# Optimization experiments

Hardware: AMD Instinct MI355X
Metric: run time of the kernel (lower is better)

The kernel has to match this reference:

```python
import jax, jax.numpy as jnp
import numpy as np


def setup_inputs() -> dict:
    key = jax.random.key(0)
    k1, k2, k3 = jax.random.split(key, 3)
    B, C_in, H, W = 32, 128, 64, 64
    C_out, KH, KW = 256, 3, 3
    x = jax.random.normal(k1, (B, C_in, H, W), dtype=jnp.float32)
    # kaiming_normal fan_out scale ~ sqrt(2 / (C_out*KH*KW)); plain normal is fine for a numeric reference
    weight = jax.random.normal(k2, (C_out, C_in, KH, KW), dtype=jnp.float32) * (2.0 / (C_out * KH * KW)) ** 0.5
    fan_in = C_in * KH * KW
    bound = 1.0 / (fan_in ** 0.5)
    bias = jax.random.uniform(k3, (C_out,), dtype=jnp.float32, minval=-bound, maxval=bound)
    return {"x": x, "weight": weight, "bias": bias}


def reference(x, weight, bias):
    # Equivalent of unfold (im2col) + matmul + fold with stride=1, padding=1:
    # a standard 2D convolution in NCHW/OIHW layout.
    out = jax.lax.conv_general_dilated(
        x, weight,
        window_strides=(1, 1),
        padding=((1, 1), (1, 1)),
        dimension_numbers=("NCHW", "OIHW", "NCHW"),
    )
    return out + bias[None, :, None, None]
```

## Files before the change

kernel.cpp:

```cpp
#include <hip/hip_runtime.h>

typedef __attribute__((ext_vector_type(4))) int   v4i;
typedef __attribute__((ext_vector_type(8))) short s8;
typedef __attribute__((ext_vector_type(4))) float f32x4;
typedef __attribute__((ext_vector_type(16))) float f32x16;

#define GLB __attribute__((address_space(1)))
#define LDS_AS __attribute__((address_space(3)))

__device__ __forceinline__ unsigned short f2bf(float f) {
  unsigned u = __builtin_bit_cast(unsigned, f);
  return (unsigned short)((u + 0x7fffu + ((u >> 16) & 1u)) >> 16);
}

__global__ void prep(const float* __restrict__ x, const float* __restrict__ w,
                     unsigned int* __restrict__ xw, unsigned short* __restrict__ ww) {
  int t = threadIdx.x;
  if (blockIdx.x >= 2048) {
    int o = (blockIdx.x - 2048) * 256 + t;
    int tap = o >> 15;
    int c   = (o >> 13) & 3;
    int cog = (o >> 10) & 7;
    int kk  = (o >> 9) & 1;
    int lh  = (o >> 8) & 1;
    int l31 = (o >> 3) & 31;
    int e   = o & 7;
    int co = cog * 32 + l31;
    int ci = c * 32 + kk * 16 + lh * 8 + e;
    ww[o] = f2bf(w[(co * 128 + ci) * 9 + tap]);
    return;
  }
  __shared__ float tile[128][65];
  int bid = blockIdx.x;
  int b = bid >> 6, h = bid & 63;
  {
    int wcol4 = (t & 15) * 4, cl = t >> 4;
    const float* src = x + ((size_t)(b * 128) * 64 + h) * 64 + wcol4;
#pragma unroll
    for (int j = 0; j < 8; ++j) {
      int ci = j * 16 + cl;
      f32x4 v = *(const f32x4*)(src + (size_t)ci * 4096);
      tile[ci][wcol4 + 0] = v[0];
      tile[ci][wcol4 + 1] = v[1];
      tile[ci][wcol4 + 2] = v[2];
      tile[ci][wcol4 + 3] = v[3];
    }
  }
  unsigned int* dst = xw + (size_t)((b * 66 + h + 1) * 66) * 64;
  if (t < 128) {
    int col = (t >> 6) ? 65 : 0;
    dst[(size_t)col * 64 + (t & 63)] = 0u;
  }
  if (h == 0 || h == 63) {
    unsigned int* rb = xw + (size_t)(b * 66 + (h == 0 ? 0 : 65)) * 66 * 64;
    for (int j = t; j < 66 * 64; j += 256) rb[j] = 0u;
  }
  __syncthreads();
  {
    int ci2 = (t & 63) * 2, wl = t >> 6;
#pragma unroll
    for (int j = 0; j < 16; ++j) {
      int wcol = j * 4 + wl;
      unsigned p = (unsigned)f2bf(tile[ci2][wcol]) |
                   ((unsigned)f2bf(tile[ci2 + 1][wcol]) << 16);
      dst[(size_t)(wcol + 1) * 64 + (t & 63)] = p;
    }
  }
}

__global__ __launch_bounds__(256, 4) void conv_mfma(
    const unsigned short* __restrict__ xw, const unsigned short* __restrict__ ww,
    const float* __restrict__ bias, float* __restrict__ out) {
  __shared__ unsigned short Xl[204 * 128];
  const int tid = threadIdx.x;
  const int lane = tid & 63;
  const int l31 = lane & 31, lh = lane >> 5;
  const int mw = tid >> 6;
  int bid = blockIdx.x;
  bid = (bid & 7) * 512 + (bid >> 3);
  const int co_t = bid & 1;
  const int pt = bid >> 1;
  const int b = pt >> 6, h0 = pt & 63;
  const unsigned xlb = (unsigned)(unsigned long long)((LDS_AS void*)Xl);

  {
    const char* xbase = (const char*)xw;
#pragma unroll
    for (int it = 0; it < 13; ++it) {
      int s = tid + it * 256;
      if (s < 3264) {
        int q = s >> 4, p = s & 15;
        int u = p ^ (q & 15);
        int rr = q / 68, cc = q - rr * 68;
        if (cc > 65) cc = 65;
        unsigned src = (unsigned)((b * 66 + h0 + rr) * 66 + cc) * 256u + (unsigned)u * 16u;
        __builtin_amdgcn_global_load_lds((const GLB unsigned int*)(xbase + src),
                                         (LDS_AS unsigned int*)&Xl[s * 8], 16, 0, 0);
      }
    }
  }

  f32x16 acc[2];
#pragma unroll
  for (int n = 0; n < 2; ++n)
#pragma unroll
    for (int e = 0; e < 16; ++e) acc[n][e] = 0.f;

  v4i areg[3][2];
  v4i breg[2][4];
  const unsigned abyte = (unsigned)(co_t * 8192 + mw * 2048 + lane * 16);

  #define ALOAD_ASM(slot, step)                                               \
    do {                                                                      \
      unsigned _wo = (unsigned)(step) * 16384u + abyte;                       \
      asm volatile("global_load_dwordx4 %0, %1, %2 offset:0"                  \
                   : "=v"(areg[slot][0]) : "v"(_wo), "s"(ww));                \
      asm volatile("global_load_dwordx4 %0, %1, %2 offset:1024"               \
                   : "=v"(areg[slot][1]) : "v"(_wo), "s"(ww));                \
    } while (0)

  #define BLOAD_ASM(slot, S)                                                  \
    do {                                                                      \
      const int _t = (S) >> 2, _c = (S) & 3;                                  \
      const int _kh = _t / 3, _kw = _t - _kh * 3;                             \
      const int _q0 = _kh * 68 + _kw + l31;                                   \
      const int _xq = (_q0 & 15) ^ lh;             \
      unsigned _a0 = xlb + (unsigned)((_q0 << 8) + (((_c * 4) ^ _xq) << 4));  \
      unsigned _a1 = xlb + (unsigned)((_q0 << 8) + (((_c * 4 + 2) ^ _xq) << 4)); \
      asm volatile("ds_read_b128 %0, %1" : "=v"(breg[slot][0]) : "v"(_a0));   \
      asm volatile("ds_read_b128 %0, %1 offset:8192"                          \
                   : "=v"(breg[slot][1]) : "v"(_a0));                         \
      asm volatile("ds_read_b128 %0, %1" : "=v"(breg[slot][2]) : "v"(_a1));   \
      asm volatile("ds_read_b128 %0, %1 offset:8192"                          \
                   : "=v"(breg[slot][3]) : "v"(_a1));                         \
    } while (0)

  #define KSTEP(S)                                                            \
    do {                                                                      \
      const int _s = (S);                                                     \
      if (_s < 34) ALOAD_ASM((_s + 2) % 3, _s + 2);                           \
      if (_s < 35) BLOAD_ASM((_s + 1) & 1, _s + 1);                           \
      if (_s < 34)                                                            \
        asm volatile("s_waitcnt vmcnt(4) lgkmcnt(4)" ::: "memory");           \
      else if (_s == 34)                                                      \
        asm volatile("s_waitcnt vmcnt(2) lgkmcnt(4)" ::: "memory");           \
      else                                                                    \
        asm volatile("s_waitcnt vmcnt(0) lgkmcnt(0)" ::: "memory");           \
      __builtin_amdgcn_sched_barrier(0);                                      \
      const int _cs = _s % 3, _bs = _s & 1;                                   \
      __builtin_amdgcn_s_setprio(1);                                          \
      acc[0] = __builtin_amdgcn_mfma_f32_32x32x16_bf16(__builtin_bit_cast(s8, areg[_cs][0]), __builtin_bit_cast(s8, breg[_bs][0]), acc[0], 0, 0, 0); \
      acc[1] = __builtin_amdgcn_mfma_f32_32x32x16_bf16(__builtin_bit_cast(s8, areg[_cs][0]), __builtin_bit_cast(s8, breg[_bs][1]), acc[1], 0, 0, 0); \
      acc[0] = __builtin_amdgcn_mfma_f32_32x32x16_bf16(__builtin_bit_cast(s8, areg[_cs][1]), __builtin_bit_cast(s8, breg[_bs][2]), acc[0], 0, 0, 0); \
      acc[1] = __builtin_amdgcn_mfma_f32_32x32x16_bf16(__builtin_bit_cast(s8, areg[_cs][1]), __builtin_bit_cast(s8, breg[_bs][3]), acc[1], 0, 0, 0); \
      __builtin_amdgcn_s_setprio(0);                                          \
    } while (0)

  ALOAD_ASM(0, 0);
  ALOAD_ASM(1, 1);
  asm volatile("s_waitcnt vmcnt(4)" ::: "memory");
  __builtin_amdgcn_sched_barrier(0);
  __builtin_amdgcn_s_barrier();
  BLOAD_ASM(0, 0);

#pragma unroll
  for (int s = 0; s < 36; ++s) KSTEP(s);

#pragma unroll
  for (int rq = 0; rq < 4; ++rq) {
    const int cob = co_t * 128 + mw * 32 + 8 * rq + 4 * lh;
    const f32x4 bi = *(const f32x4*)(bias + cob);
#pragma unroll
    for (int n = 0; n < 2; ++n) {
      const int wc = n * 32 + l31;
      size_t base = ((size_t)(b * 256 + cob) * 64 + h0) * 64 + wc;
#pragma unroll
      for (int e = 0; e < 4; ++e)
        out[base + (size_t)e * 4096] = acc[n][rq * 4 + e] + bi[e];
    }
  }
}

__global__ void conv_naive(const float* __restrict__ x, const float* __restrict__ w,
                           const float* __restrict__ bias, float* __restrict__ out) {
  int i = blockIdx.x * 256 + threadIdx.x;
  int wc = i & 63, h = (i >> 6) & 63, co = (i >> 12) & 255, b = i >> 20;
  float s = bias[co];
  for (int ci = 0; ci < 128; ++ci)
#pragma unroll
    for (int kh = 0; kh < 3; ++kh) {
      int hh = h + kh - 1;
      if ((unsigned)hh >= 64u) continue;
#pragma unroll
      for (int kw = 0; kw < 3; ++kw) {
        int wg = wc + kw - 1;
        if ((unsigned)wg >= 64u) continue;
        s += x[((b * 128 + ci) * 64 + hh) * 64 + wg] *
             w[((co * 128 + ci) * 3 + kh) * 3 + kw];
      }
    }
  out[i] = s;
}

extern "C" void kernel_launch(void* const* d_in, const int* in_sizes, int n_in,
                              void* d_out, int out_size, void* d_ws, size_t ws_size,
                              hipStream_t stream) {
  const float* x    = (const float*)d_in[0];
  const float* w    = (const float*)d_in[1];
  const float* bias = (const float*)d_in[2];
  float* out = (float*)d_out;

  const size_t X_OFF  = 1ull << 20;
  const size_t XBYTES = 32ull * 66 * 66 * 128 * 2;
  const size_t NEED   = X_OFF + XBYTES;

  if (ws_size >= NEED) {
    unsigned short* ww = (unsigned short*)d_ws;
    unsigned short* xq = (unsigned short*)((char*)d_ws + X_OFF);
    hipLaunchKernelGGL(prep, dim3(3200), dim3(256), 0, stream, x, w,
                       (unsigned int*)xq, ww);
    hipLaunchKernelGGL(conv_mfma, dim3(4096), dim3(256), 0, stream, xq, ww, bias, out);
  } else {
    hipLaunchKernelGGL(conv_naive, dim3(131072), dim3(256), 0, stream, x, w, bias, out);
  }
}
```

Baseline: 98.49 us.

## Enlarge conv tile to 256 channels by 256 pixels with double-buffered LDS staging

The MFMA conv kernel now has each 512-thread block compute all 256 output channels for four output rows (256 pixels). Both weights and the input halo slices are staged into a double-buffered LDS ring via direct global-to-LDS loads, one k-tile ahead. Each wave computes a 128x64 sub-tile with 4x2 MFMA accumulators, fed by LDS fragment reads interleaved with the MFMAs. This is meant to raise operand reuse and cut redundant global traffic for weights and inputs. In exchange it uses more registers, a full 128KB of LDS, two barriers per k-step, and only 512 blocks.

```diff
diff --git a/kernel.cpp b/kernel.cpp
--- a/kernel.cpp
+++ b/kernel.cpp
@@ -68,117 +68,151 @@
   }
 }
 
-__global__ __launch_bounds__(256, 4) void conv_mfma(
+__global__ __launch_bounds__(512, 2) void conv_mfma(
     const unsigned short* __restrict__ xw, const unsigned short* __restrict__ ww,
     const float* __restrict__ bias, float* __restrict__ out) {
-  __shared__ unsigned short Xl[204 * 128];
+  __shared__ unsigned short Xl[65536];
   const int tid = threadIdx.x;
   const int lane = tid & 63;
   const int l31 = lane & 31, lh = lane >> 5;
-  const int mw = tid >> 6;
+  const int wid = tid >> 6;
+  const int wm = wid >> 2;
+  const int wn = wid & 3;
   int bid = blockIdx.x;
-  bid = (bid & 7) * 512 + (bid >> 3);
-  const int co_t = bid & 1;
-  const int pt = bid >> 1;
-  const int b = pt >> 6, h0 = pt & 63;
+  bid = (bid & 7) * 64 + (bid >> 3);
+  const int b = bid >> 4, h0 = (bid & 15) << 2;
   const unsigned xlb = (unsigned)(unsigned long long)((LDS_AS void*)Xl);
-
-  {
-    const char* xbase = (const char*)xw;
-#pragma unroll
-    for (int it = 0; it < 13; ++it) {
-      int s = tid + it * 256;
-      if (s < 3264) {
-        int q = s >> 4, p = s & 15;
-        int u = p ^ (q & 15);
-        int rr = q / 68, cc = q - rr * 68;
-        if (cc > 65) cc = 65;
-        unsigned src = (unsigned)((b * 66 + h0 + rr) * 66 + cc) * 256u + (unsigned)u * 16u;
-        __builtin_amdgcn_global_load_lds((const GLB unsigned int*)(xbase + src),
-                                         (LDS_AS unsigned int*)&Xl[s * 8], 16, 0, 0);
+  const char* wwb = (const char*)ww;
+  const char* xqb = (const char*)xw;
+
+  unsigned ia[4], pbx[4];
+#pragma unroll
+  for (int j = 0; j < 4; ++j) {
+    int s = tid + j * 512;
+    int cog = s >> 8, cp = (s >> 7) & 1, kk = (s >> 6) & 1;
+    int lhs = (s >> 5) & 1, l31s = s & 31;
+    ia[j] = (unsigned)((cog * 1024 + kk * 512 + lhs * 256 + l31s * 8) * 2 + cp * 16384);
+    int pix = s & 255, u = s >> 8;
+    int pr = pix >> 6, pc = pix & 63;
+    pbx[j] = (unsigned)(((b * 66 + h0 + pr) * 66 + pc) * 256 + u * 16);
+  }
+
+  #define STAGE(kt)                                                           \
+    do {                                                                      \
+      const int _tap = (kt) >> 1, _ch = (kt) & 1;                             \
+      const unsigned _ka = (unsigned)(_tap * 65536 + _ch * 32768);            \
+      const int _kh = _tap / 3, _kw = _tap - _kh * 3;                         \
+      const unsigned _kb = (unsigned)((_kh * 66 + _kw) * 256 + _ch * 128);    \
+      const int _abh = ((kt) & 1) * 16384;                  \
+      _Pragma("unroll")                                                       \
+      for (int _j = 0; _j < 4; ++_j)                                          \
+        __builtin_amdgcn_global_load_lds(                                     \
+            (const GLB unsigned int*)(wwb + _ka + ia[_j]),                    \
+            (LDS_AS unsigned int*)&Xl[_abh + (tid + _j * 512) * 8], 16, 0, 0);\
+      _Pragma("unroll")                                                       \
+      for (int _j = 0; _j < 4; ++_j)                                          \
+        __builtin_amdgcn_global_load_lds(                                     \
+            (const GLB unsigned int*)(xqb + _kb + pbx[_j]),                   \
+            (LDS_AS unsigned int*)&Xl[32768 + _abh + (tid + _j * 512) * 8],   \
+            16, 0, 0);                                                        \
+    } while (0)
+
+  f32x16 acc[4][2];
+#pragma unroll
+  for (int m = 0; m < 4; ++m)
+#pragma unroll
+    for (int n = 0; n < 2; ++n)
+#pragma unroll
+      for (int e = 0; e < 16; ++e) acc[m][n][e] = 0.f;
+
+  v4i aph[2][4];
+  v4i bph[2][2];
+  const unsigned ard = (unsigned)(wm * 16384 + lane * 16);
+  const unsigned brd = (unsigned)(65536 + lh * 4096 + (wn * 64 + l31) * 16);
+
+  #define APH(sl, p, bo)                                                      \
+    do {                                                                      \
+      unsigned _a = xlb + (bo) + ard + (unsigned)((p) * 1024);                \
+      asm volatile("ds_read_b128 %0, %1"              : "=v"(aph[sl][0]) : "v"(_a)); \
+      asm volatile("ds_read_b128 %0, %1 offset:4096"  : "=v"(aph[sl][1]) : "v"(_a)); \
+      asm volatile("ds_read_b128 %0, %1 offset:8192"  : "=v"(aph[sl][2]) : "v"(_a)); \
+      asm volatile("ds_read_b128 %0, %1 offset:12288" : "=v"(aph[sl][3]) : "v"(_a)); \
+    } while (0)
+
+  #define BPH(sl, p, bo)                                                      \
+    do {                                                                      \
+      unsigned _b = xlb + (bo) + brd + (unsigned)((p) * 8192);                \
+      asm volatile("ds_read_b128 %0, %1"             : "=v"(bph[sl][0]) : "v"(_b)); \
+      asm volatile("ds_read_b128 %0, %1 offset:512"  : "=v"(bph[sl][1]) : "v"(_b)); \
+    } while (0)
+
+  #define MFMA1(d, af, bf) \
+    d = __builtin_amdgcn_mfma_f32_32x32x16_bf16(__builtin_bit_cast(s8, af), \
+                                                __builtin_bit_cast(s8, bf), d, 0, 0, 0)
+  #define MFMA8(sl)                                                           \
+    do {                                                                      \
+      MFMA1(acc[0][0], aph[sl][0], bph[sl][0]);                               \
+      MFMA1(acc[1][0], aph[sl][1], bph[sl][0]);                               \
+      MFMA1(acc[2][0], aph[sl][2], bph[sl][0]);                               \
+      MFMA1(acc[3][0], aph[sl][3], bph[sl][0]);                               \
+      MFMA1(acc[0][1], aph[sl][0], bph[sl][1]);                               \
+      MFMA1(acc[1][1], aph[sl][1], bph[sl][1]);                               \
+      MFMA1(acc[2][1], aph[sl][2], bph[sl][1]);                               \
+      MFMA1(acc[3][1], aph[sl][3], bph[sl][1]);                               \
+    } while (0)
+
+  #define SB __builtin_amdgcn_sched_barrier(0)
+  #define PRIO1 __builtin_amdgcn_s_setprio(1)
+  #define PRIO0 __builtin_amdgcn_s_setprio(0)
+
+  STAGE(0);
+
+#pragma unroll
+  for (int kt = 0; kt < 18; ++kt) {
+    const unsigned bo = (unsigned)((kt & 1) * 32768);
+    if (kt < 17) {
+      STAGE(kt + 1);
+      asm volatile("s_waitcnt vmcnt(8)" ::: "memory");
+    } else {
+      asm volatile("s_waitcnt vmcnt(0)" ::: "memory");
+    }
+    SB;
+    __builtin_amdgcn_s_barrier();
+
+    APH(0, 0, bo); BPH(0, 0, bo);
+    APH(1, 1, bo); BPH(1, 1, bo);
+    asm volatile("s_waitcnt lgkmcnt(6)" ::: "memory");
+    SB; PRIO1; MFMA8(0); PRIO0;
+
+    APH(0, 2, bo); BPH(0, 2, bo);
+    asm volatile("s_waitcnt lgkmcnt(6)" ::: "memory");
+    SB; PRIO1; MFMA8(1); PRIO0;
+
+    APH(1, 3, bo); BPH(1, 3, bo);
+    asm volatile("s_waitcnt lgkmcnt(6)" ::: "memory");
+    SB; PRIO1; MFMA8(0); PRIO0;
+
+    asm volatile("s_waitcnt lgkmcnt(0)" ::: "memory");
+    SB; PRIO1; MFMA8(1); PRIO0;
+    __builtin_amdgcn_s_barrier();
+  }
+
+#pragma unroll
+  for (int m = 0; m < 4; ++m)
+#pragma unroll
+    for (int rq = 0; rq < 4; ++rq) {
+      const int cob = wm * 128 + m * 32 + 8 * rq + 4 * lh;
+      const f32x4 bi = *(const f32x4*)(bias + cob);
+#pragma unroll
+      for (int n = 0; n < 2; ++n) {
+        const int pix = wn * 64 + n * 32 + l31;
+        const int pr = pix >> 6, pc = pix & 63;
+        size_t base = ((size_t)(b * 256 + cob) * 64 + (h0 + pr)) * 64 + pc;
+#pragma unroll
+        for (int e = 0; e < 4; ++e)
+          out[base + (size_t)e * 4096] = acc[m][n][rq * 4 + e] + bi[e];
       }
     }
-  }
-
-  f32x16 acc[2];
-#pragma unroll
-  for (int n = 0; n < 2; ++n)
-#pragma unroll
-    for (int e = 0; e < 16; ++e) acc[n][e] = 0.f;
-
-  v4i areg[3][2];
-  v4i breg[2][4];
-  const unsigned abyte = (unsigned)(co_t * 8192 + mw * 2048 + lane * 16);
-
-  #define ALOAD_ASM(slot, step)                                               \
-    do {                                                                      \
-      unsigned _wo = (unsigned)(step) * 16384u + abyte;                       \
-      asm volatile("global_load_dwordx4 %0, %1, %2 offset:0"                  \
-                   : "=v"(areg[slot][0]) : "v"(_wo), "s"(ww));                \
-      asm volatile("global_load_dwordx4 %0, %1, %2 offset:1024"               \
-                   : "=v"(areg[slot][1]) : "v"(_wo), "s"(ww));                \
-    } while (0)
-
-  #define BLOAD_ASM(slot, S)                                                  \
-    do {                                                                      \
-      const int _t = (S) >> 2, _c = (S) & 3;                                  \
-      const int _kh = _t / 3, _kw = _t - _kh * 3;                             \
-      const int _q0 = _kh * 68 + _kw + l31;                                   \
-      const int _xq = (_q0 & 15) ^ lh;             \
-      unsigned _a0 = xlb + (unsigned)((_q0 << 8) + (((_c * 4) ^ _xq) << 4));  \
-      unsigned _a1 = xlb + (unsigned)((_q0 << 8) + (((_c * 4 + 2) ^ _xq) << 4)); \
-      asm volatile("ds_read_b128 %0, %1" : "=v"(breg[slot][0]) : "v"(_a0));   \
-      asm volatile("ds_read_b128 %0, %1 offset:8192"                          \
-                   : "=v"(breg[slot][1]) : "v"(_a0));                         \
-      asm volatile("ds_read_b128 %0, %1" : "=v"(breg[slot][2]) : "v"(_a1));   \
-      asm volatile("ds_read_b128 %0, %1 offset:8192"                          \
-                   : "=v"(breg[slot][3]) : "v"(_a1));                         \
-    } while (0)
-
-  #define KSTEP(S)                                                            \
-    do {                                                                      \
-      const int _s = (S);                                                     \
-      if (_s < 34) ALOAD_ASM((_s + 2) % 3, _s + 2);                           \
-      if (_s < 35) BLOAD_ASM((_s + 1) & 1, _s + 1);                           \
-      if (_s < 34)                                                            \
-        asm volatile("s_waitcnt vmcnt(4) lgkmcnt(4)" ::: "memory");           \
-      else if (_s == 34)                                                      \
-        asm volatile("s_waitcnt vmcnt(2) lgkmcnt(4)" ::: "memory");           \
-      else                                                                    \
-        asm volatile("s_waitcnt vmcnt(0) lgkmcnt(0)" ::: "memory");           \
-      __builtin_amdgcn_sched_barrier(0);                                      \
-      const int _cs = _s % 3, _bs = _s & 1;                                   \
-      __builtin_amdgcn_s_setprio(1);                                          \
-      acc[0] = __builtin_amdgcn_mfma_f32_32x32x16_bf16(__builtin_bit_cast(s8, areg[_cs][0]), __builtin_bit_cast(s8, breg[_bs][0]), acc[0], 0, 0, 0); \
-      acc[1] = __builtin_amdgcn_mfma_f32_32x32x16_bf16(__builtin_bit_cast(s8, areg[_cs][0]), __builtin_bit_cast(s8, breg[_bs][1]), acc[1], 0, 0, 0); \
-      acc[0] = __builtin_amdgcn_mfma_f32_32x32x16_bf16(__builtin_bit_cast(s8, areg[_cs][1]), __builtin_bit_cast(s8, breg[_bs][2]), acc[0], 0, 0, 0); \
-      acc[1] = __builtin_amdgcn_mfma_f32_32x32x16_bf16(__builtin_bit_cast(s8, areg[_cs][1]), __builtin_bit_cast(s8, breg[_bs][3]), acc[1], 0, 0, 0); \
-      __builtin_amdgcn_s_setprio(0);                                          \
-    } while (0)
-
-  ALOAD_ASM(0, 0);
-  ALOAD_ASM(1, 1);
-  asm volatile("s_waitcnt vmcnt(4)" ::: "memory");
-  __builtin_amdgcn_sched_barrier(0);
-  __builtin_amdgcn_s_barrier();
-  BLOAD_ASM(0, 0);
-
-#pragma unroll
-  for (int s = 0; s < 36; ++s) KSTEP(s);
-
-#pragma unroll
-  for (int rq = 0; rq < 4; ++rq) {
-    const int cob = co_t * 128 + mw * 32 + 8 * rq + 4 * lh;
-    const f32x4 bi = *(const f32x4*)(bias + cob);
-#pragma unroll
-    for (int n = 0; n < 2; ++n) {
-      const int wc = n * 32 + l31;
-      size_t base = ((size_t)(b * 256 + cob) * 64 + h0) * 64 + wc;
-#pragma unroll
-      for (int e = 0; e < 4; ++e)
-        out[base + (size_t)e * 4096] = acc[n][rq * 4 + e] + bi[e];
-    }
-  }
 }
 
 __global__ void conv_naive(const float* __restrict__ x, const float* __restrict__ w,
@@ -219,7 +253,7 @@
     unsigned short* xq = (unsigned short*)((char*)d_ws + X_OFF);
     hipLaunchKernelGGL(prep, dim3(3200), dim3(256), 0, stream, x, w,
                        (unsigned int*)xq, ww);
-    hipLaunchKernelGGL(conv_mfma, dim3(4096), dim3(256), 0, stream, xq, ww, bias, out);
+    hipLaunchKernelGGL(conv_mfma, dim3(512), dim3(512), 0, stream, xq, ww, bias, out);
   } else {
     hipLaunchKernelGGL(conv_naive, dim3(131072), dim3(256), 0, stream, x, w, bias, out);
   }
```

After: 120.9 us. 1.23x slower.
